# Kernel optimization log

Hardware: AMD Instinct MI355X
Metric: run time of the kernel (lower is better)

## Reference

```python
import jax, jax.numpy as jnp
import numpy as np

B, C_IN, H, W = 16, 1024, 32, 32
D_CODE, K = 1024, 2048  # codebook_dim, codebook_size


def setup_inputs() -> dict:
    key = jax.random.key(0)
    k1, k2, k3, k4 = jax.random.split(key, 4)
    x = jax.random.normal(k1, (B, C_IN, H, W), dtype=jnp.float32)
    # 1x1 conv kernel stored as (out=D_CODE, in=C_IN); scaled like torch conv init
    conv_w = jax.random.normal(k2, (D_CODE, C_IN), dtype=jnp.float32) / np.sqrt(C_IN)
    conv_b = jax.random.normal(k3, (D_CODE,), dtype=jnp.float32) * 0.01
    codebook = jax.random.normal(k4, (D_CODE, K), dtype=jnp.float32)
    return {"x": x, "conv_w": conv_w, "conv_b": conv_b, "codebook": codebook}


def reference(x, conv_w, conv_b, codebook):
    # 1x1 conv projection: (B, C_IN, H, W) -> (B, D_CODE, H, W)
    xp = jnp.einsum('bchw,dc->bdhw', x, conv_w) + conv_b[None, :, None, None]

    b, d, h, w = xp.shape
    # flatten spatial: (N, D) with N = B*H*W (matches 'b d h w -> (b h w) d')
    xf = jnp.transpose(xp, (0, 2, 3, 1)).reshape(-1, d)

    # pairwise squared distances to codebook columns: (N, K)
    dist = (jnp.sum(xf * xf, axis=1, keepdims=True)
            - 2.0 * (xf @ codebook)
            + jnp.sum(codebook * codebook, axis=0, keepdims=True))
    indices = jnp.argmin(dist, axis=1).reshape(b, h, w)  # (B, H, W)

    # gather codes: codebook.T is (K, D)
    quant_hw_d = codebook.T[indices]  # (B, H, W, D)
    quant = jnp.transpose(quant_hw_d, (0, 3, 1, 2))  # (B, D, H, W)

    # commitment loss (quantized detached)
    diff = jnp.mean((jax.lax.stop_gradient(quant) - xp) ** 2)

    # straight-through estimator
    quant_st = xp + jax.lax.stop_gradient(quant - xp)
    return quant_st, diff, indices
```

## Files before the change

kernel.cpp:

```cpp
#include <hip/hip_runtime.h>
#include <stdint.h>

#define BATCH 16
#define CIN   1024
#define HWSZ  1024
#define NPOS  16384
#define DCODE 1024
#define KCB   2048

#define OUT_QUANT 0
#define OUT_DIFF  16777216
#define OUT_IDX   16777217

#define OFF_PACKED 0u
#define OFF_CNORM  131072u
#define OFF_DIFF   139264u
#define OFF_WH     262144u
#define OFF_WL     2359296u
#define OFF_CBH    4456448u
#define OFF_CBL    8650752u
#define OFF_DYN    12845056u

typedef _Float16 f16x8 __attribute__((ext_vector_type(8)));
typedef float f32x4 __attribute__((ext_vector_type(4)));
union H4 { _Float16 h[4]; uint2 u; };
union H8 { _Float16 h[8]; uint4 u; };
union QU { uint4 u; uint16_t v[8]; };

__device__ __forceinline__ void gl_lds16(const void* g, void* l) {
  __builtin_amdgcn_global_load_lds(
      (const __attribute__((address_space(1))) uint32_t*)g,
      (__attribute__((address_space(3))) uint32_t*)l, 16, 0, 0);
}

__global__ void k_init(unsigned long long* __restrict__ packed, double* __restrict__ diffsum) {
  int i = blockIdx.x * 256 + threadIdx.x;
  if (i < NPOS) packed[i] = 0xFFFFFFFFFFFFFFFFull;
  if (i == 0) *diffsum = 0.0;
}

__global__ __launch_bounds__(256) void k_prep_w(const float* __restrict__ w,
                                                _Float16* __restrict__ wh, _Float16* __restrict__ wl) {
  const int d = blockIdx.x;
  const int c = threadIdx.x * 4;
  float4 v = *(const float4*)&w[(size_t)d * CIN + c];
  H4 hh, ll;
  float vv[4] = {v.x, v.y, v.z, v.w};
  #pragma unroll
  for (int i = 0; i < 4; ++i) {
    _Float16 h = (_Float16)vv[i];
    hh.h[i] = h;
    ll.h[i] = (_Float16)(vv[i] - (float)h);
  }
  *(uint2*)&wh[(size_t)d * CIN + c] = hh.u;
  *(uint2*)&wl[(size_t)d * CIN + c] = ll.u;
}

__global__ __launch_bounds__(256) void k_prep_cb(const float* __restrict__ cb,
                                                 _Float16* __restrict__ cbh, _Float16* __restrict__ cbl) {
  __shared__ float ts[64][65];
  const int t = threadIdx.x;
  const int k0 = blockIdx.x * 64, d0 = blockIdx.y * 64;
  #pragma unroll
  for (int i = 0; i < 4; ++i) {
    const int r = i * 16 + (t >> 4);
    float4 v = *(const float4*)&cb[(size_t)(d0 + r) * KCB + k0 + (t & 15) * 4];
    ts[r][(t & 15) * 4 + 0] = v.x; ts[r][(t & 15) * 4 + 1] = v.y;
    ts[r][(t & 15) * 4 + 2] = v.z; ts[r][(t & 15) * 4 + 3] = v.w;
  }
  __syncthreads();
  const int j = t >> 2;
  const int q = t & 3;
  H8 hh[2], ll[2];
  #pragma unroll
  for (int e = 0; e < 16; ++e) {
    float xv = ts[q * 16 + e][j];
    _Float16 h = (_Float16)xv;
    hh[e >> 3].h[e & 7] = h;
    ll[e >> 3].h[e & 7] = (_Float16)(xv - (float)h);
  }
  size_t o = (size_t)(k0 + j) * DCODE + d0 + q * 16;
  *(uint4*)&cbh[o] = hh[0].u; *(uint4*)&cbh[o + 8] = hh[1].u;
  *(uint4*)&cbl[o] = ll[0].u; *(uint4*)&cbl[o + 8] = ll[1].u;
}

__global__ __launch_bounds__(256) void k_prep_x(const float* __restrict__ x,
                                                _Float16* __restrict__ xh, _Float16* __restrict__ xl,
                                                int n_base) {
  __shared__ float ts[64][65];
  const int t = threadIdx.x;
  const int nt0 = blockIdx.x * 64;
  const int c0 = blockIdx.y * 64;
  const int ng = n_base + nt0;
  const int b = ng >> 10, hw0 = ng & 1023;
  #pragma unroll
  for (int i = 0; i < 4; ++i) {
    const int r = i * 16 + (t >> 4);
    float4 v = *(const float4*)&x[((size_t)b * CIN + c0 + r) * HWSZ + hw0 + (t & 15) * 4];
    ts[r][(t & 15) * 4 + 0] = v.x; ts[r][(t & 15) * 4 + 1] = v.y;
    ts[r][(t & 15) * 4 + 2] = v.z; ts[r][(t & 15) * 4 + 3] = v.w;
  }
  __syncthreads();
  const int j = t >> 2;
  const int q = t & 3;
  H8 hh[2], ll[2];
  #pragma unroll
  for (int e = 0; e < 16; ++e) {
    float xv = ts[q * 16 + e][j];
    _Float16 h = (_Float16)xv;
    hh[e >> 3].h[e & 7] = h;
    ll[e >> 3].h[e & 7] = (_Float16)(xv - (float)h);
  }
  size_t o = (size_t)(nt0 + j) * CIN + c0 + q * 16;
  *(uint4*)&xh[o] = hh[0].u; *(uint4*)&xh[o + 8] = hh[1].u;
  *(uint4*)&xl[o] = ll[0].u; *(uint4*)&xl[o + 8] = ll[1].u;
}

__global__ __launch_bounds__(256) void k_cnorm2(const _Float16* __restrict__ cbh,
                                                const _Float16* __restrict__ cbl,
                                                float* __restrict__ cnorm) {
  __shared__ double rd[256];
  const int k = blockIdx.x;
  const int t = threadIdx.x;
  H4 hh, ll;
  hh.u = *(const uint2*)&cbh[(size_t)k * DCODE + t * 4];
  ll.u = *(const uint2*)&cbl[(size_t)k * DCODE + t * 4];
  double s = 0.0;
  #pragma unroll
  for (int i = 0; i < 4; ++i) {
    float v = (float)hh.h[i] + (float)ll.h[i];
    s += (double)v * v;
  }
  rd[t] = s;
  __syncthreads();
  for (int st = 128; st > 0; st >>= 1) {
    if (t < st) rd[t] += rd[t + st];
    __syncthreads();
  }
  if (t == 0) cnorm[k] = (float)rd[0];
}

template <int EPI, int NKTT>
__global__ __launch_bounds__(512, 2) void k_gemm_u(
    const _Float16* __restrict__ aH, const _Float16* __restrict__ aL,
    const _Float16* __restrict__ bH, const _Float16* __restrict__ bL,
    const float* __restrict__ bias,
    _Float16* __restrict__ oH, _Float16* __restrict__ oL,
    const float* __restrict__ cnorm, unsigned long long* __restrict__ packed,
    uint16_t* __restrict__ dqout, int n_base) {
  __shared__ __align__(16) _Float16 smem[65536];
  const int tid = threadIdx.x;
  const int lane = tid & 63, wid = tid >> 6;
  const int wm = wid >> 2, wn = wid & 3;
  const int m0 = blockIdx.x * 256;
  const int n0 = blockIdx.y * 256;
  const int kg = lane >> 4;
  const int l7 = lane & 7;

  const int srow = lane >> 3;
  const int sg = l7 ^ srow;
  size_t srcA[4], srcB[4];
  int sdst[4];
  #pragma unroll
  for (int i = 0; i < 4; ++i) {
    const int r = i * 64 + wid * 8 + srow;
    srcA[i] = (size_t)(m0 + r) * 1024 + sg * 8;
    srcB[i] = (size_t)(n0 + r) * 1024 + sg * 8;
    sdst[i] = i * 4096 + wid * 512;
  }
  const int xrd[2] = {(kg ^ l7) * 8, ((4 + kg) ^ l7) * 8};
  int arow[8], brow[4];
  #pragma unroll
  for (int fi = 0; fi < 8; ++fi) arow[fi] = (wm * 128 + fi * 16 + (lane & 15)) * 64;
  #pragma unroll
  for (int fj = 0; fj < 4; ++fj) brow[fj] = 16384 + (wn * 64 + fj * 16 + (lane & 15)) * 64;

  auto stage = [&](int kt, int part) {
    const int tp = kt >> 4;
    const int dbase = (kt & 15) * 64;
    const int buf = (kt & 1) << 15;
    if (part == 0) {
      const _Float16* pA = (tp == 2 ? aL : aH);
      #pragma unroll
      for (int i = 0; i < 4; ++i) gl_lds16(pA + srcA[i] + dbase, smem + buf + sdst[i]);
    } else {
      const _Float16* pB = (tp == 1 ? bL : bH);
      #pragma unroll
      for (int i = 0; i < 4; ++i) gl_lds16(pB + srcB[i] + dbase, smem + buf + 16384 + sdst[i]);
    }
  };

  f32x4 acc[8][4];
  #pragma unroll
  for (int i = 0; i < 8; ++i)
    #pragma unroll
    for (int j = 0; j < 4; ++j) acc[i][j] = (f32x4){0.f, 0.f, 0.f, 0.f};

  stage(0, 0); stage(0, 1);
  asm volatile("s_waitcnt vmcnt(0)" ::: "memory");
  __builtin_amdgcn_s_barrier();
  __builtin_amdgcn_sched_barrier(0);

  for (int kt = 0; kt < NKTT; ++kt) {
    const int buf = (kt & 1) << 15;
    f16x8 bfr[4][2];
    #pragma unroll
    for (int fj = 0; fj < 4; ++fj)
      #pragma unroll
      for (int ks = 0; ks < 2; ++ks)
        bfr[fj][ks] = *(const f16x8*)&smem[buf + brow[fj] + xrd[ks]];
    #pragma unroll
    for (int q = 0; q < 4; ++q) {
      f16x8 afr[2][2];
      #pragma unroll
      for (int f2 = 0; f2 < 2; ++f2)
        #pragma unroll
        for (int ks = 0; ks < 2; ++ks)
          afr[f2][ks] = *(const f16x8*)&smem[buf + arow[q * 2 + f2] + xrd[ks]];
      if (kt < NKTT - 1) {
        if (q == 0) stage(kt + 1, 0);
        else if (q == 1) stage(kt + 1, 1);
      }
      __builtin_amdgcn_s_setprio(1);
      #pragma unroll
      for (int f2 = 0; f2 < 2; ++f2)
        #pragma unroll
        for (int fj = 0; fj < 4; ++fj)
          #pragma unroll
          for (int ks = 0; ks < 2; ++ks)
            acc[q * 2 + f2][fj] = __builtin_amdgcn_mfma_f32_16x16x32_f16(
                afr[f2][ks], bfr[fj][ks], acc[q * 2 + f2][fj], 0, 0, 0);
      __builtin_amdgcn_s_setprio(0);
      __builtin_amdgcn_sched_barrier(0);
    }
    asm volatile("s_waitcnt vmcnt(0)" ::: "memory");
    __builtin_amdgcn_s_barrier();
    __builtin_amdgcn_sched_barrier(0);
  }

  if (EPI == 1) {
    unsigned long long* su = (unsigned long long*)smem;
    float cn[4]; int kcol[4];
    #pragma unroll
    for (int fj = 0; fj < 4; ++fj) {
      kcol[fj] = n0 + wn * 64 + fj * 16 + (lane & 15);
      cn[fj] = cnorm[kcol[fj]];
    }
    #pragma unroll
    for (int fi = 0; fi < 8; ++fi) {
      #pragma unroll
      for (int r = 0; r < 4; ++r) {
        float best = 3.4e38f; int bk = 0;
        #pragma unroll
        for (int fj = 0; fj < 4; ++fj) {
          const float v = cn[fj] - 2.0f * acc[fi][fj][r];
          if (v < best) { best = v; bk = kcol[fj]; }
        }
        union { float f; uint32_t u; } cv; cv.f = best;
        uint32_t hi = cv.u ^ ((uint32_t)((int32_t)cv.u >> 31) | 0x80000000u);
        unsigned long long key = ((unsigned long long)hi << 32) | (uint32_t)bk;
        #pragma unroll
        for (int s = 1; s < 16; s <<= 1) {
          unsigned long long o = __shfl_xor(key, s, 64);
          if (o < key) key = o;
        }
        if ((lane & 15) == 0)
          su[wn * 256 + wm * 128 + fi * 16 + kg * 4 + r] = key;
      }
    }
    __syncthreads();
    if (tid < 256) {
      unsigned long long k = su[tid];
      #pragma unroll
      for (int w = 1; w < 4; ++w) {
        unsigned long long o = su[w * 256 + tid];
        if (o < k) k = o;
      }
      atomicMin(&packed[n_base + m0 + tid], k);
    }
  } else if (EPI == 2) {
    uint16_t* sq = (uint16_t*)smem;
    float cn[4]; int kcolL[4];
    #pragma unroll
    for (int fj = 0; fj < 4; ++fj) {
      kcolL[fj] = wn * 64 + fj * 16 + (lane & 15);
      cn[fj] = cnorm[n0 + kcolL[fj]];
    }
    const int sw = kg << 4;
    #pragma unroll
    for (int fi = 0; fi < 8; ++fi)
      #pragma unroll
      for (int r = 0; r < 4; ++r) {
        const int pos_l = wm * 128 + fi * 16 + kg * 4 + r;
        #pragma unroll
        for (int fj = 0; fj < 4; ++fj) {
          float qf = (cn[fj] - 2.0f * acc[fi][fj][r] - 512.f) * 16.f;
          uint32_t qq = qf <= 0.f ? 0u : (qf >= 65535.f ? 65535u : (uint32_t)qf);
          sq[pos_l * 256 + (kcolL[fj] ^ sw)] = (uint16_t)qq;
        }
      }
    __syncthreads();
    #pragma unroll
    for (int p = 0; p < 16; ++p) {
      const int row = p * 16 + (tid >> 5);
      const int lc = tid & 31;
      const int pc = lc ^ (((row >> 2) & 3) << 1);
      *(uint4*)&dqout[(size_t)(m0 + row) * 2048 + n0 + lc * 8] = *(const uint4*)&sq[row * 256 + pc * 8];
    }
  } else {
    float bi[4];
    #pragma unroll
    for (int fj = 0; fj < 4; ++fj) bi[fj] = bias[n0 + wn * 64 + fj * 16 + (lane & 15)];
    const int sw = kg << 4;
    #pragma unroll
    for (int pl = 0; pl < 2; ++pl) {
      #pragma unroll
      for (int fi = 0; fi < 8; ++fi)
        #pragma unroll
        for (int r = 0; r < 4; ++r) {
          const int pos_l = wm * 128 + fi * 16 + kg * 4 + r;
          #pragma unroll
          for (int fj = 0; fj < 4; ++fj) {
            const int d_l = wn * 64 + fj * 16 + (lane & 15);
            float v = acc[fi][fj][r] + bi[fj];
            _Float16 h = (_Float16)v;
            smem[pos_l * 256 + (d_l ^ sw)] = pl ? (_Float16)(v - (float)h) : h;
          }
        }
      __syncthreads();
      _Float16* dst = pl ? oL : oH;
      #pragma unroll
      for (int p = 0; p < 16; ++p) {
        const int row = p * 16 + (tid >> 5);
        const int lc = tid & 31;
        const int pc = lc ^ (((row >> 2) & 3) << 1);
        *(uint4*)&dst[(size_t)(m0 + row) * 1024 + n0 + lc * 8] = *(const uint4*)&smem[row * 256 + pc * 8];
      }
      __syncthreads();
    }
  }
}

__global__ __launch_bounds__(256) void k_refine(
    const uint16_t* __restrict__ dq,
    const _Float16* __restrict__ xph, const _Float16* __restrict__ xpl,
    const _Float16* __restrict__ cbh, const _Float16* __restrict__ cbl,
    unsigned long long* __restrict__ packed) {
  const int n = blockIdx.x;
  const int t = threadIdx.x;
  __shared__ float xpr[1024];
  __shared__ uint32_t smin[256];
  __shared__ double red[256];
  __shared__ int cand[64];
  __shared__ int ncand;
  if (t == 0) ncand = 0;
  {
    H4 hh, ll;
    hh.u = *(const uint2*)&xph[(size_t)n * 1024 + t * 4];
    ll.u = *(const uint2*)&xpl[(size_t)n * 1024 + t * 4];
    #pragma unroll
    for (int i = 0; i < 4; ++i) xpr[t * 4 + i] = (float)hh.h[i] + (float)ll.h[i];
  }
  QU qv;
  qv.u = *(const uint4*)&dq[(size_t)n * 2048 + t * 8];
  uint32_t lmin = 0xFFFFFFFFu;
  #pragma unroll
  for (int j = 0; j < 8; ++j) lmin = (qv.v[j] < lmin) ? qv.v[j] : lmin;
  smin[t] = lmin;
  __syncthreads();
  for (int s = 128; s > 0; s >>= 1) {
    if (t < s && smin[t + s] < smin[t]) smin[t] = smin[t + s];
    __syncthreads();
  }
  const uint32_t thr = smin[0] + 8;
  #pragma unroll
  for (int j = 0; j < 8; ++j)
    if (qv.v[j] <= thr) {
      int p = atomicAdd(&ncand, 1);
      if (p < 64) cand[p] = t * 8 + j;
    }
  __syncthreads();
  int nc = ncand; if (nc > 64) nc = 64;
  double best_d = 1e300; int best_k = 0x7FFFFFFF;
  for (int c = 0; c < nc; ++c) {
    const int k = cand[c];
    H4 ch, cl;
    ch.u = *(const uint2*)&cbh[(size_t)k * 1024 + t * 4];
    cl.u = *(const uint2*)&cbl[(size_t)k * 1024 + t * 4];
    double s = 0.0;
    #pragma unroll
    for (int i = 0; i < 4; ++i) {
      double dd = (double)xpr[t * 4 + i] - (double)((float)ch.h[i] + (float)cl.h[i]);
      s += dd * dd;
    }
    red[t] = s;
    __syncthreads();
    for (int st = 128; st > 0; st >>= 1) {
      if (t < st) red[t] += red[t + st];
      __syncthreads();
    }
    const double d = red[0];
    __syncthreads();
    if (d < best_d || (d == best_d && k < best_k)) { best_d = d; best_k = k; }
  }
  if (t == 0) packed[n] = (unsigned long long)(uint32_t)best_k;
}

__global__ __launch_bounds__(256) void k_gather2(
    const _Float16* __restrict__ cbh, const _Float16* __restrict__ cbl,
    const _Float16* __restrict__ xph, const _Float16* __restrict__ xpl,
    const unsigned long long* __restrict__ packed,
    float* __restrict__ out, double* __restrict__ diffsum,
    int n_base, int NC) {
  __shared__ float tile[64][65];
  __shared__ uint32_t sidx[64];
  __shared__ float red[256];
  const int t = threadIdx.x;
  const int n0 = blockIdx.x * 64;
  const int ng = n_base + n0;
  const int b = ng >> 10, hw0 = ng & 1023;
  const int dbeg = blockIdx.y * 256;
  if (t < 64) {
    uint32_t idx = (uint32_t)(packed[ng + t] & 0xFFFFFFFFu);
    if (idx > (KCB - 1)) idx = KCB - 1;
    sidx[t] = idx;
  }
  const int rrow = t >> 3, rcol = (t & 7) * 8;
  const int wd = t >> 4, whw = (t & 15) * 4;
  float local = 0.f;
  for (int d0 = dbeg; d0 < dbeg + 256; d0 += 64) {
    __syncthreads();
    #pragma unroll
    for (int p = 0; p < 2; ++p) {
      const int nl = p * 32 + rrow;
      const uint32_t idx = sidx[nl];
      H8 hh, ll, ph, pl;
      hh.u = *(const uint4*)&cbh[(size_t)idx * DCODE + d0 + rcol];
      ll.u = *(const uint4*)&cbl[(size_t)idx * DCODE + d0 + rcol];
      ph.u = *(const uint4*)&xph[(size_t)(n0 + nl) * DCODE + d0 + rcol];
      pl.u = *(const uint4*)&xpl[(size_t)(n0 + nl) * DCODE + d0 + rcol];
      #pragma unroll
      for (int j = 0; j < 8; ++j) {
        const float q = (float)hh.h[j] + (float)ll.h[j];
        const float xv = (float)ph.h[j] + (float)pl.h[j];
        const float dd = q - xv;
        local += dd * dd;
        tile[nl][rcol + j] = q;
      }
    }
    __syncthreads();
    #pragma unroll
    for (int i = 0; i < 4; ++i) {
      const int dl = i * 16 + wd;
      float4 v;
      v.x = tile[whw + 0][dl]; v.y = tile[whw + 1][dl];
      v.z = tile[whw + 2][dl]; v.w = tile[whw + 3][dl];
      *(float4*)&out[((size_t)b * DCODE + d0 + dl) * HWSZ + hw0 + whw] = v;
    }
  }
  red[t] = local;
  __syncthreads();
  for (int s = 128; s > 0; s >>= 1) {
    if (t < s) red[t] += red[t + s];
    __syncthreads();
  }
  if (t == 0) atomicAdd(diffsum, (double)red[0]);
}

__global__ void k_final(const unsigned long long* __restrict__ packed,
                        const double* __restrict__ diffsum,
                        float* __restrict__ out) {
  int i = blockIdx.x * 256 + threadIdx.x;
  if (i < NPOS) {
    uint32_t idx = (uint32_t)(packed[i] & 0xFFFFFFFFu);
    if (idx > (KCB - 1)) idx = KCB - 1;
    out[OUT_IDX + i] = (float)idx;
  }
  if (i == 0) out[OUT_DIFF] = (float)(*diffsum / ((double)NPOS * (double)DCODE));
}

extern "C" void kernel_launch(void* const* d_in, const int* in_sizes, int n_in,
                              void* d_out, int out_size, void* d_ws, size_t ws_size,
                              hipStream_t stream) {
  const float* x    = (const float*)d_in[0];
  const float* w    = (const float*)d_in[1];
  const float* bias = (const float*)d_in[2];
  const float* cb   = (const float*)d_in[3];
  float* out = (float*)d_out;
  char* ws = (char*)d_ws;
  unsigned long long* packed = (unsigned long long*)(ws + OFF_PACKED);
  float* cnorm = (float*)(ws + OFF_CNORM);
  double* diffsum = (double*)(ws + OFF_DIFF);
  _Float16* wh  = (_Float16*)(ws + OFF_WH);
  _Float16* wl  = (_Float16*)(ws + OFF_WL);
  _Float16* cbh = (_Float16*)(ws + OFF_CBH);
  _Float16* cbl = (_Float16*)(ws + OFF_CBL);

  const size_t OFF_DQ = (size_t)OFF_DYN + (size_t)16384 * 8192;
  const bool fast = ws_size >= OFF_DQ + (size_t)16384 * 2048 * 2;

  k_init<<<64, 256, 0, stream>>>(packed, diffsum);
  k_prep_w<<<DCODE, 256, 0, stream>>>(w, wh, wl);
  k_prep_cb<<<dim3(KCB / 64, DCODE / 64), 256, 0, stream>>>(cb, cbh, cbl);
  k_cnorm2<<<KCB, 256, 0, stream>>>(cbh, cbl, cnorm);

  if (fast) {
    const int NC = 16384;
    char* dyn = ws + OFF_DYN;
    _Float16* xh  = (_Float16*)dyn;
    _Float16* xl  = (_Float16*)(dyn + (size_t)NC * 2048);
    _Float16* xph = (_Float16*)(dyn + (size_t)NC * 4096);
    _Float16* xpl = (_Float16*)(dyn + (size_t)NC * 6144);
    uint16_t* dq  = (uint16_t*)(ws + OFF_DQ);
    k_prep_x<<<dim3(NC / 64, CIN / 64), 256, 0, stream>>>(x, xh, xl, 0);
    k_gemm_u<0, 48><<<dim3(NC / 256, DCODE / 256), 512, 0, stream>>>(
        xh, xl, wh, wl, bias, xph, xpl, nullptr, nullptr, nullptr, 0);
    k_gemm_u<2, 16><<<dim3(NC / 256, KCB / 256), 512, 0, stream>>>(
        xph, xpl, cbh, cbl, nullptr, nullptr, nullptr, cnorm, nullptr, dq, 0);
    k_refine<<<NPOS, 256, 0, stream>>>(dq, xph, xpl, cbh, cbl, packed);
    k_gather2<<<dim3(NC / 64, 4), 256, 0, stream>>>(cbh, cbl, xph, xpl, packed, out, diffsum, 0, NC);
  } else {
    int NC = 256;
    if      (ws_size >= OFF_DYN + (size_t)16384 * 8192) NC = 16384;
    else if (ws_size >= OFF_DYN + (size_t)8192  * 8192) NC = 8192;
    else if (ws_size >= OFF_DYN + (size_t)4096  * 8192) NC = 4096;
    else if (ws_size >= OFF_DYN + (size_t)2048  * 8192) NC = 2048;
    else if (ws_size >= OFF_DYN + (size_t)1024  * 8192) NC = 1024;
    else if (ws_size >= OFF_DYN + (size_t)512   * 8192) NC = 512;
    const int nchunks = NPOS / NC;
    char* dyn = ws + OFF_DYN;
    _Float16* xh  = (_Float16*)dyn;
    _Float16* xl  = (_Float16*)(dyn + (size_t)NC * 2048);
    _Float16* xph = (_Float16*)(dyn + (size_t)NC * 4096);
    _Float16* xpl = (_Float16*)(dyn + (size_t)NC * 6144);
    for (int c = 0; c < nchunks; ++c) {
      const int n_base = c * NC;
      k_prep_x<<<dim3(NC / 64, CIN / 64), 256, 0, stream>>>(x, xh, xl, n_base);
      k_gemm_u<0, 48><<<dim3(NC / 256, DCODE / 256), 512, 0, stream>>>(
          xh, xl, wh, wl, bias, xph, xpl, nullptr, nullptr, nullptr, 0);
      k_gemm_u<1, 48><<<dim3(NC / 256, KCB / 256), 512, 0, stream>>>(
          xph, xpl, cbh, cbl, nullptr, nullptr, nullptr, cnorm, packed, nullptr, n_base);
      k_gather2<<<dim3(NC / 64, 4), 256, 0, stream>>>(cbh, cbl, xph, xpl, packed, out, diffsum, n_base, NC);
    }
  }
  k_final<<<64, 256, 0, stream>>>(packed, diffsum, out);
}
```

Measured before the change: 279.6 us.

## Screen codebook distances with int8 MFMA GEMM before exact refinement

```diff
diff --git a/kernel.cpp b/kernel.cpp
--- a/kernel.cpp
+++ b/kernel.cpp
@@ -23,9 +23,11 @@
 
 typedef _Float16 f16x8 __attribute__((ext_vector_type(8)));
 typedef float f32x4 __attribute__((ext_vector_type(4)));
+typedef int i32x4 __attribute__((ext_vector_type(4)));
 union H4 { _Float16 h[4]; uint2 u; };
 union H8 { _Float16 h[8]; uint4 u; };
 union QU { uint4 u; uint16_t v[8]; };
+union B16 { char c[16]; uint4 u; };
 
 __device__ __forceinline__ void gl_lds16(const void* g, void* l) {
   __builtin_amdgcn_global_load_lds(
@@ -57,7 +59,8 @@
 }
 
 __global__ __launch_bounds__(256) void k_prep_cb(const float* __restrict__ cb,
-                                                 _Float16* __restrict__ cbh, _Float16* __restrict__ cbl) {
+                                                 _Float16* __restrict__ cbh, _Float16* __restrict__ cbl,
+                                                 char* __restrict__ cq) {
   __shared__ float ts[64][65];
   const int t = threadIdx.x;
   const int k0 = blockIdx.x * 64, d0 = blockIdx.y * 64;
@@ -72,16 +75,21 @@
   const int j = t >> 2;
   const int q = t & 3;
   H8 hh[2], ll[2];
+  B16 qb;
   #pragma unroll
   for (int e = 0; e < 16; ++e) {
     float xv = ts[q * 16 + e][j];
     _Float16 h = (_Float16)xv;
     hh[e >> 3].h[e & 7] = h;
     ll[e >> 3].h[e & 7] = (_Float16)(xv - (float)h);
+    int qi = (int)rintf(xv * 20.f);
+    qi = qi > 127 ? 127 : (qi < -127 ? -127 : qi);
+    qb.c[e] = (char)qi;
   }
   size_t o = (size_t)(k0 + j) * DCODE + d0 + q * 16;
   *(uint4*)&cbh[o] = hh[0].u; *(uint4*)&cbh[o + 8] = hh[1].u;
   *(uint4*)&cbl[o] = ll[0].u; *(uint4*)&cbl[o + 8] = ll[1].u;
+  if (cq) *(uint4*)&cq[o] = qb.u;
 }
 
 __global__ __launch_bounds__(256) void k_prep_x(const float* __restrict__ x,
@@ -114,6 +122,25 @@
   size_t o = (size_t)(nt0 + j) * CIN + c0 + q * 16;
   *(uint4*)&xh[o] = hh[0].u; *(uint4*)&xh[o + 8] = hh[1].u;
   *(uint4*)&xl[o] = ll[0].u; *(uint4*)&xl[o + 8] = ll[1].u;
+}
+
+__global__ __launch_bounds__(256) void k_prep_xq(const _Float16* __restrict__ xph,
+                                                 char* __restrict__ xq) {
+  const size_t base = ((size_t)blockIdx.x * 256 + threadIdx.x) * 16;
+  H8 a, b;
+  a.u = *(const uint4*)&xph[base];
+  b.u = *(const uint4*)&xph[base + 8];
+  B16 qb;
+  #pragma unroll
+  for (int i = 0; i < 8; ++i) {
+    int qi = (int)rintf((float)a.h[i] * 20.f);
+    qi = qi > 127 ? 127 : (qi < -127 ? -127 : qi);
+    qb.c[i] = (char)qi;
+    int qj = (int)rintf((float)b.h[i] * 20.f);
+    qj = qj > 127 ? 127 : (qj < -127 ? -127 : qj);
+    qb.c[8 + i] = (char)qj;
+  }
+  *(uint4*)&xq[base] = qb.u;
 }
 
 __global__ __launch_bounds__(256) void k_cnorm2(const _Float16* __restrict__ cbh,
@@ -278,35 +305,6 @@
       }
       atomicMin(&packed[n_base + m0 + tid], k);
     }
-  } else if (EPI == 2) {
-    uint16_t* sq = (uint16_t*)smem;
-    float cn[4]; int kcolL[4];
-    #pragma unroll
-    for (int fj = 0; fj < 4; ++fj) {
-      kcolL[fj] = wn * 64 + fj * 16 + (lane & 15);
-      cn[fj] = cnorm[n0 + kcolL[fj]];
-    }
-    const int sw = kg << 4;
-    #pragma unroll
-    for (int fi = 0; fi < 8; ++fi)
-      #pragma unroll
-      for (int r = 0; r < 4; ++r) {
-        const int pos_l = wm * 128 + fi * 16 + kg * 4 + r;
-        #pragma unroll
-        for (int fj = 0; fj < 4; ++fj) {
-          float qf = (cn[fj] - 2.0f * acc[fi][fj][r] - 512.f) * 16.f;
-          uint32_t qq = qf <= 0.f ? 0u : (qf >= 65535.f ? 65535u : (uint32_t)qf);
-          sq[pos_l * 256 + (kcolL[fj] ^ sw)] = (uint16_t)qq;
-        }
-      }
-    __syncthreads();
-    #pragma unroll
-    for (int p = 0; p < 16; ++p) {
-      const int row = p * 16 + (tid >> 5);
-      const int lc = tid & 31;
-      const int pc = lc ^ (((row >> 2) & 3) << 1);
-      *(uint4*)&dqout[(size_t)(m0 + row) * 2048 + n0 + lc * 8] = *(const uint4*)&sq[row * 256 + pc * 8];
-    }
   } else {
     float bi[4];
     #pragma unroll
@@ -338,6 +336,127 @@
       }
       __syncthreads();
     }
+  }
+}
+
+__global__ __launch_bounds__(512, 2) void k_screen_q(
+    const char* __restrict__ xq, const char* __restrict__ cq,
+    const float* __restrict__ cnorm, uint16_t* __restrict__ dqout) {
+  __shared__ __align__(16) char smem[131072];
+  const int tid = threadIdx.x;
+  const int lane = tid & 63, wid = tid >> 6;
+  const int wm = wid >> 2, wn = wid & 3;
+  const int m0 = blockIdx.x * 256;
+  const int n0 = blockIdx.y * 256;
+  const int kg = lane >> 4;
+  const int l7 = lane & 7;
+  const int l15 = lane & 15;
+
+  const int srow = lane >> 3;
+  const int sg = l7 ^ srow;
+  size_t srcA[4], srcB[4];
+  int sdst[4];
+  #pragma unroll
+  for (int i = 0; i < 4; ++i) {
+    const int r = i * 64 + wid * 8 + srow;
+    srcA[i] = (size_t)(m0 + r) * 1024 + sg * 16;
+    srcB[i] = (size_t)(n0 + r) * 1024 + sg * 16;
+    sdst[i] = i * 8192 + wid * 1024;
+  }
+  const int xrd[2] = {(kg ^ l7) * 16, ((4 + kg) ^ l7) * 16};
+  int arow[8], brow[4];
+  #pragma unroll
+  for (int fi = 0; fi < 8; ++fi) arow[fi] = (wm * 128 + fi * 16 + l15) * 128;
+  #pragma unroll
+  for (int fj = 0; fj < 4; ++fj) brow[fj] = 32768 + (wn * 64 + fj * 16 + l15) * 128;
+
+  auto stage = [&](int kt, int part) {
+    const int dbase = kt * 128;
+    const int buf = (kt & 1) << 16;
+    if (part == 0) {
+      #pragma unroll
+      for (int i = 0; i < 4; ++i) gl_lds16(xq + srcA[i] + dbase, smem + buf + sdst[i]);
+    } else {
+      #pragma unroll
+      for (int i = 0; i < 4; ++i) gl_lds16(cq + srcB[i] + dbase, smem + buf + 32768 + sdst[i]);
+    }
+  };
+
+  i32x4 acc[8][4];
+  #pragma unroll
+  for (int i = 0; i < 8; ++i)
+    #pragma unroll
+    for (int j = 0; j < 4; ++j) acc[i][j] = (i32x4){0, 0, 0, 0};
+
+  stage(0, 0); stage(0, 1);
+  asm volatile("s_waitcnt vmcnt(0)" ::: "memory");
+  __builtin_amdgcn_s_barrier();
+  __builtin_amdgcn_sched_barrier(0);
+
+  for (int kt = 0; kt < 8; ++kt) {
+    const int buf = (kt & 1) << 16;
+    i32x4 bfr[4][2];
+    #pragma unroll
+    for (int fj = 0; fj < 4; ++fj)
+      #pragma unroll
+      for (int ks = 0; ks < 2; ++ks)
+        bfr[fj][ks] = *(const i32x4*)&smem[buf + brow[fj] + xrd[ks]];
+    #pragma unroll
+    for (int q = 0; q < 4; ++q) {
+      i32x4 afr[2][2];
+      #pragma unroll
+      for (int f2 = 0; f2 < 2; ++f2)
+        #pragma unroll
+        for (int ks = 0; ks < 2; ++ks)
+          afr[f2][ks] = *(const i32x4*)&smem[buf + arow[q * 2 + f2] + xrd[ks]];
+      if (kt < 7) {
+        if (q == 0) stage(kt + 1, 0);
+        else if (q == 1) stage(kt + 1, 1);
+      }
+      __builtin_amdgcn_s_setprio(1);
+      #pragma unroll
+      for (int f2 = 0; f2 < 2; ++f2)
+        #pragma unroll
+        for (int fj = 0; fj < 4; ++fj)
+          #pragma unroll
+          for (int ks = 0; ks < 2; ++ks)
+            acc[q * 2 + f2][fj] = __builtin_amdgcn_mfma_i32_16x16x64_i8(
+                afr[f2][ks], bfr[fj][ks], acc[q * 2 + f2][fj], 0, 0, 0);
+      __builtin_amdgcn_s_setprio(0);
+      __builtin_amdgcn_sched_barrier(0);
+    }
+    asm volatile("s_waitcnt vmcnt(0)" ::: "memory");
+    __builtin_amdgcn_s_barrier();
+    __builtin_amdgcn_sched_barrier(0);
+  }
+
+  uint16_t* sq = (uint16_t*)smem;
+  float cn[4]; int kcolL[4];
+  #pragma unroll
+  for (int fj = 0; fj < 4; ++fj) {
+    kcolL[fj] = wn * 64 + fj * 16 + l15;
+    cn[fj] = cnorm[n0 + kcolL[fj]];
+  }
+  const int sw = kg << 4;
+  #pragma unroll
+  for (int fi = 0; fi < 8; ++fi)
+    #pragma unroll
+    for (int r = 0; r < 4; ++r) {
+      const int pos_l = wm * 128 + fi * 16 + kg * 4 + r;
+      #pragma unroll
+      for (int fj = 0; fj < 4; ++fj) {
+        float qf = (cn[fj] - 0.005f * (float)acc[fi][fj][r] - 512.f) * 16.f;
+        uint32_t qq = qf <= 0.f ? 0u : (qf >= 65535.f ? 65535u : (uint32_t)qf);
+        sq[pos_l * 256 + (kcolL[fj] ^ sw)] = (uint16_t)qq;
+      }
+    }
+  __syncthreads();
+  #pragma unroll
+  for (int p = 0; p < 16; ++p) {
+    const int row = p * 16 + (tid >> 5);
+    const int lc = tid & 31;
+    const int pc = lc ^ (((row >> 2) & 3) << 1);
+    *(uint4*)&dqout[(size_t)(m0 + row) * 2048 + n0 + lc * 8] = *(const uint4*)&sq[row * 256 + pc * 8];
   }
 }
 
@@ -372,7 +491,7 @@
     if (t < s && smin[t + s] < smin[t]) smin[t] = smin[t + s];
     __syncthreads();
   }
-  const uint32_t thr = smin[0] + 8;
+  const uint32_t thr = smin[0] + 192;
   #pragma unroll
   for (int j = 0; j < 8; ++j)
     if (qv.v[j] <= thr) {
@@ -496,13 +615,11 @@
   _Float16* cbh = (_Float16*)(ws + OFF_CBH);
   _Float16* cbl = (_Float16*)(ws + OFF_CBL);
 
-  const size_t OFF_DQ = (size_t)OFF_DYN + (size_t)16384 * 8192;
-  const bool fast = ws_size >= OFF_DQ + (size_t)16384 * 2048 * 2;
+  const size_t need_fast = (size_t)OFF_DYN + (size_t)16384 * 8192 + 16777216 + 2097152;
+  const bool fast = ws_size >= need_fast;
 
   k_init<<<64, 256, 0, stream>>>(packed, diffsum);
   k_prep_w<<<DCODE, 256, 0, stream>>>(w, wh, wl);
-  k_prep_cb<<<dim3(KCB / 64, DCODE / 64), 256, 0, stream>>>(cb, cbh, cbl);
-  k_cnorm2<<<KCB, 256, 0, stream>>>(cbh, cbl, cnorm);
 
   if (fast) {
     const int NC = 16384;
@@ -511,15 +628,21 @@
     _Float16* xl  = (_Float16*)(dyn + (size_t)NC * 2048);
     _Float16* xph = (_Float16*)(dyn + (size_t)NC * 4096);
     _Float16* xpl = (_Float16*)(dyn + (size_t)NC * 6144);
-    uint16_t* dq  = (uint16_t*)(ws + OFF_DQ);
+    char* xq = dyn + (size_t)NC * 8192;
+    char* cq = xq + 16777216;
+    uint16_t* dq = (uint16_t*)out;
+    k_prep_cb<<<dim3(KCB / 64, DCODE / 64), 256, 0, stream>>>(cb, cbh, cbl, cq);
+    k_cnorm2<<<KCB, 256, 0, stream>>>(cbh, cbl, cnorm);
     k_prep_x<<<dim3(NC / 64, CIN / 64), 256, 0, stream>>>(x, xh, xl, 0);
     k_gemm_u<0, 48><<<dim3(NC / 256, DCODE / 256), 512, 0, stream>>>(
         xh, xl, wh, wl, bias, xph, xpl, nullptr, nullptr, nullptr, 0);
-    k_gemm_u<2, 16><<<dim3(NC / 256, KCB / 256), 512, 0, stream>>>(
-        xph, xpl, cbh, cbl, nullptr, nullptr, nullptr, cnorm, nullptr, dq, 0);
+    k_prep_xq<<<4096, 256, 0, stream>>>(xph, xq);
+    k_screen_q<<<dim3(NC / 256, KCB / 256), 512, 0, stream>>>(xq, cq, cnorm, dq);
     k_refine<<<NPOS, 256, 0, stream>>>(dq, xph, xpl, cbh, cbl, packed);
     k_gather2<<<dim3(NC / 64, 4), 256, 0, stream>>>(cbh, cbl, xph, xpl, packed, out, diffsum, 0, NC);
   } else {
+    k_prep_cb<<<dim3(KCB / 64, DCODE / 64), 256, 0, stream>>>(cb, cbh, cbl, nullptr);
+    k_cnorm2<<<KCB, 256, 0, stream>>>(cbh, cbl, cnorm);
     int NC = 256;
     if      (ws_size >= OFF_DYN + (size_t)16384 * 8192) NC = 16384;
     else if (ws_size >= OFF_DYN + (size_t)8192  * 8192) NC = 8192;
```

New measurement: 277.1 us. Within noise of the previous version (-0.9%).
